# Kernel optimization log

Hardware: AMD Instinct MI355X
Metric: run time of the kernel (lower is better)

Reference implementation:

```python
import jax, jax.numpy as jnp
import numpy as np

HIDDEN_DIM = 2048
NUM_EXPERTS = 64
TOP_K = 2
NUM_TOKENS = 16384


def setup_inputs() -> dict:
    key = jax.random.key(0)
    kx, kw, kb = jax.random.split(key, 3)
    X = jax.random.normal(kx, (NUM_TOKENS, HIDDEN_DIM), dtype=jnp.float32)
    # nn.Linear(hidden_dim, num_experts): weight [num_experts, hidden_dim], bias [num_experts]
    bound = 1.0 / np.sqrt(HIDDEN_DIM)
    W = jax.random.uniform(kw, (NUM_EXPERTS, HIDDEN_DIM), minval=-bound, maxval=bound, dtype=jnp.float32)
    b = jax.random.uniform(kb, (NUM_EXPERTS,), minval=-bound, maxval=bound, dtype=jnp.float32)
    return {"X": X, "W": W, "b": b}


def reference(X, W, b):
    # router_logits = gate(X): [T, E]
    router_logits = jnp.einsum("th,eh->te", X, W) + b
    # softmax in float32 (matches dtype=torch.float)
    routing_probs = jax.nn.softmax(router_logits.astype(jnp.float32), axis=-1)
    # top-k over experts: [T, K]
    router_weights, selected_experts = jax.lax.top_k(routing_probs, TOP_K)
    # renormalize over selected experts (sum cast to X.dtype, result stays fp32 math)
    denom = jnp.sum(router_weights, axis=-1, keepdims=True).astype(X.dtype)
    router_weights = router_weights / denom
    # one-hot expert mask: [T, K, E], int64 like F.one_hot
    expert_mask = jax.nn.one_hot(selected_experts, NUM_EXPERTS, dtype=jnp.int32)
    return (router_logits, router_weights, selected_experts, expert_mask)
```

## Files before the change

### kernel.cpp

```cpp
#include <hip/hip_runtime.h>
#include <math.h>

constexpr int T_TOK = 16384;
constexpr int HDIM  = 2048;
constexpr int NEXP  = 64;
constexpr int TPB   = 64;
constexpr int NWAVE = 8;
constexpr int KPW   = HDIM / NWAVE;
constexpr int KSTEP = 32;
constexpr int NKS   = KPW / KSTEP;

typedef __attribute__((ext_vector_type(8))) short v8s;
typedef __attribute__((ext_vector_type(4))) float v4f;

#define MFMA_BF16 __builtin_amdgcn_mfma_f32_16x16x32_bf16

static __device__ __forceinline__ void split3(float x, unsigned short& h,
                                              unsigned short& m, unsigned short& l)
{
    unsigned u0 = __float_as_uint(x);
    h = (unsigned short)(u0 >> 16);
    float r1 = x - __uint_as_float(u0 & 0xFFFF0000u);
    unsigned u1 = __float_as_uint(r1);
    m = (unsigned short)(u1 >> 16);
    float r2 = r1 - __uint_as_float(u1 & 0xFFFF0000u);
    l = (unsigned short)(__float_as_uint(r2) >> 16);
}

static __device__ __forceinline__ void frag3(const float4& x0, const float4& x1,
                                             v8s& h, v8s& m, v8s& l)
{
    unsigned short sh, sm, sl;
    split3(x0.x, sh, sm, sl); h[0]=(short)sh; m[0]=(short)sm; l[0]=(short)sl;
    split3(x0.y, sh, sm, sl); h[1]=(short)sh; m[1]=(short)sm; l[1]=(short)sl;
    split3(x0.z, sh, sm, sl); h[2]=(short)sh; m[2]=(short)sm; l[2]=(short)sl;
    split3(x0.w, sh, sm, sl); h[3]=(short)sh; m[3]=(short)sm; l[3]=(short)sl;
    split3(x1.x, sh, sm, sl); h[4]=(short)sh; m[4]=(short)sm; l[4]=(short)sl;
    split3(x1.y, sh, sm, sl); h[5]=(short)sh; m[5]=(short)sm; l[5]=(short)sl;
    split3(x1.z, sh, sm, sl); h[6]=(short)sh; m[6]=(short)sm; l[6]=(short)sl;
    split3(x1.w, sh, sm, sl); h[7]=(short)sh; m[7]=(short)sm; l[7]=(short)sl;
}

static __device__ __forceinline__ int swz_e(int tok, int e) {
    return e ^ (((tok >> 2) & 1) << 4);
}

__global__ __launch_bounds__(512, 2)
void moe_router_mfma(const float* __restrict__ X,
                     const float* __restrict__ Wg,
                     const float* __restrict__ Bg,
                     float* __restrict__ out)
{
    __shared__ float red[4][TPB][NEXP];

    const int tid  = threadIdx.x;
    const int lane = tid & 63;
    const int wv   = tid >> 6;
    const int r16  = lane & 15;
    const int q    = lane >> 4;
    const int tok0 = blockIdx.x * TPB;

    const float* pA = X  + (size_t)(tok0 + r16) * HDIM + wv * KPW + q * 8;
    const float* pB = Wg + (size_t)r16 * HDIM + wv * KPW + q * 8;

    v4f acc[4][4];
#pragma unroll
    for (int mt = 0; mt < 4; ++mt)
#pragma unroll
        for (int nt = 0; nt < 4; ++nt)
            acc[mt][nt] = (v4f){0.f, 0.f, 0.f, 0.f};

    float4 a0[4], a1[4], b0[4], b1[4];
#pragma unroll
    for (int mt = 0; mt < 4; ++mt) {
        const float* p = pA + (size_t)mt * 16 * HDIM;
        a0[mt] = *(const float4*)p;
        a1[mt] = *(const float4*)(p + 4);
    }
#pragma unroll
    for (int nt = 0; nt < 4; ++nt) {
        const float* p = pB + (size_t)nt * 16 * HDIM;
        b0[nt] = *(const float4*)p;
        b1[nt] = *(const float4*)(p + 4);
    }

    for (int ks = 0; ks < NKS; ++ks) {
        v8s Ah[4], Am[4], Al[4], Bh[4], Bm[4], Bl[4];
#pragma unroll
        for (int mt = 0; mt < 4; ++mt) frag3(a0[mt], a1[mt], Ah[mt], Am[mt], Al[mt]);
#pragma unroll
        for (int nt = 0; nt < 4; ++nt) frag3(b0[nt], b1[nt], Bh[nt], Bm[nt], Bl[nt]);

        if (ks < NKS - 1) {
            const int off = (ks + 1) * KSTEP;
#pragma unroll
            for (int mt = 0; mt < 4; ++mt) {
                const float* p = pA + (size_t)mt * 16 * HDIM + off;
                a0[mt] = *(const float4*)p;
                a1[mt] = *(const float4*)(p + 4);
            }
#pragma unroll
            for (int nt = 0; nt < 4; ++nt) {
                const float* p = pB + (size_t)nt * 16 * HDIM + off;
                b0[nt] = *(const float4*)p;
                b1[nt] = *(const float4*)(p + 4);
            }
        }

#pragma unroll
        for (int mt = 0; mt < 4; ++mt)
#pragma unroll
            for (int nt = 0; nt < 4; ++nt) {
                v4f a = acc[mt][nt];
                a = MFMA_BF16(Ah[mt], Bh[nt], a, 0, 0, 0);
                a = MFMA_BF16(Ah[mt], Bm[nt], a, 0, 0, 0);
                a = MFMA_BF16(Am[mt], Bh[nt], a, 0, 0, 0);
                a = MFMA_BF16(Ah[mt], Bl[nt], a, 0, 0, 0);
                a = MFMA_BF16(Al[mt], Bh[nt], a, 0, 0, 0);
                a = MFMA_BF16(Am[mt], Bm[nt], a, 0, 0, 0);
                acc[mt][nt] = a;
            }
    }

    if (wv < 4) {
#pragma unroll
        for (int mt = 0; mt < 4; ++mt)
#pragma unroll
            for (int nt = 0; nt < 4; ++nt)
#pragma unroll
                for (int r = 0; r < 4; ++r) {
                    int tok = 16 * mt + q * 4 + r;
                    int e   = 16 * nt + r16;
                    red[wv][tok][swz_e(tok, e)] = acc[mt][nt][r];
                }
    }
    __syncthreads();
    if (wv >= 4) {
#pragma unroll
        for (int mt = 0; mt < 4; ++mt)
#pragma unroll
            for (int nt = 0; nt < 4; ++nt)
#pragma unroll
                for (int r = 0; r < 4; ++r) {
                    int tok = 16 * mt + q * 4 + r;
                    int e   = 16 * nt + r16;
                    red[wv - 4][tok][swz_e(tok, e)] += acc[mt][nt][r];
                }
    }
    __syncthreads();

    if (lane < 8) {
        const int tk = wv * 8 + lane;
        const int t  = tok0 + tk;
        float lg[NEXP];
#pragma unroll
        for (int e = 0; e < NEXP; ++e) {
            int es = swz_e(tk, e);
            lg[e] = ((red[0][tk][es] + red[1][tk][es]) +
                     (red[2][tk][es] + red[3][tk][es])) + Bg[e];
        }
        float* outL = out + (size_t)t * NEXP;
#pragma unroll
        for (int e = 0; e < NEXP; e += 4) {
            float4 v = make_float4(lg[e], lg[e+1], lg[e+2], lg[e+3]);
            *(float4*)(outL + e) = v;
        }
        float mx = lg[0];
#pragma unroll
        for (int e = 1; e < NEXP; ++e) mx = fmaxf(mx, lg[e]);
        float S = 0.f;
#pragma unroll
        for (int e = 0; e < NEXP; ++e) { lg[e] = expf(lg[e] - mx); S += lg[e]; }
#pragma unroll
        for (int e = 0; e < NEXP; ++e) lg[e] = lg[e] / S;

        float v1 = lg[0]; int i1 = 0;
        float v2 = -1.0f; int i2 = 0;
#pragma unroll
        for (int e = 1; e < NEXP; ++e) {
            float rv = lg[e];
            bool g1 = rv > v1;
            bool g2 = rv > v2;
            float nv2 = g1 ? v1 : (g2 ? rv : v2);
            int   ni2 = g1 ? i1 : (g2 ? e  : i2);
            v2 = nv2; i2 = ni2;
            v1 = g1 ? rv : v1;
            i1 = g1 ? e  : i1;
        }
        float den = v1 + v2;
        float w1 = v1 / den, w2 = v2 / den;

        float* outW = out + (size_t)T_TOK * NEXP;
        float* outS = outW + (size_t)T_TOK * 2;
        float* outM = outS + (size_t)T_TOK * 2;
        outW[2*t+0] = w1;        outW[2*t+1] = w2;
        outS[2*t+0] = (float)i1; outS[2*t+1] = (float)i2;

        float* mrow = outM + (size_t)t * 2 * NEXP;
#pragma unroll
        for (int e = 0; e < NEXP; e += 4) {
            float4 a = make_float4(e+0==i1?1.f:0.f, e+1==i1?1.f:0.f,
                                   e+2==i1?1.f:0.f, e+3==i1?1.f:0.f);
            *(float4*)(mrow + e) = a;
            float4 b = make_float4(e+0==i2?1.f:0.f, e+1==i2?1.f:0.f,
                                   e+2==i2?1.f:0.f, e+3==i2?1.f:0.f);
            *(float4*)(mrow + NEXP + e) = b;
        }
    }
}

extern "C" void kernel_launch(void* const* d_in, const int* in_sizes, int n_in,
                              void* d_out, int out_size, void* d_ws, size_t ws_size,
                              hipStream_t stream)
{
    const float* X = (const float*)d_in[0];
    const float* W = (const float*)d_in[1];
    const float* B = (const float*)d_in[2];
    float* out     = (float*)d_out;

    dim3 grid(T_TOK / TPB);
    dim3 block(512);
    hipLaunchKernelGGL(moe_router_mfma, grid, block, 0, stream, X, W, B, out);
}
```

Before: 223.5 us.

## Pre-split W into bf16 planes in a prep kernel and halve tokens per block

```diff
diff --git a/kernel.cpp b/kernel.cpp
--- a/kernel.cpp
+++ b/kernel.cpp
@@ -4,11 +4,12 @@
 constexpr int T_TOK = 16384;
 constexpr int HDIM  = 2048;
 constexpr int NEXP  = 64;
-constexpr int TPB   = 64;
+constexpr int TPB   = 32;
 constexpr int NWAVE = 8;
 constexpr int KPW   = HDIM / NWAVE;
 constexpr int KSTEP = 32;
 constexpr int NKS   = KPW / KSTEP;
+constexpr int WPLANE = NEXP * HDIM;
 
 typedef __attribute__((ext_vector_type(8))) short v8s;
 typedef __attribute__((ext_vector_type(4))) float v4f;
@@ -45,9 +46,24 @@
     return e ^ (((tok >> 2) & 1) << 4);
 }
 
+__global__ __launch_bounds__(256)
+void split_w_kernel(const float* __restrict__ W, unsigned short* __restrict__ ws)
+{
+    int i = blockIdx.x * 256 + threadIdx.x;
+    float4 v = ((const float4*)W)[i];
+    ushort4 h, m, l;
+    split3(v.x, h.x, m.x, l.x);
+    split3(v.y, h.y, m.y, l.y);
+    split3(v.z, h.z, m.z, l.z);
+    split3(v.w, h.w, m.w, l.w);
+    ((ushort4*)(ws           ))[i] = h;
+    ((ushort4*)(ws + WPLANE  ))[i] = m;
+    ((ushort4*)(ws + 2*WPLANE))[i] = l;
+}
+
 __global__ __launch_bounds__(512, 2)
 void moe_router_mfma(const float* __restrict__ X,
-                     const float* __restrict__ Wg,
+                     const unsigned short* __restrict__ Ws,
                      const float* __restrict__ Bg,
                      float* __restrict__ out)
 {
@@ -60,71 +76,71 @@
     const int q    = lane >> 4;
     const int tok0 = blockIdx.x * TPB;
 
-    const float* pA = X  + (size_t)(tok0 + r16) * HDIM + wv * KPW + q * 8;
-    const float* pB = Wg + (size_t)r16 * HDIM + wv * KPW + q * 8;
-
-    v4f acc[4][4];
-#pragma unroll
-    for (int mt = 0; mt < 4; ++mt)
+    const float* pA = X + (size_t)(tok0 + r16) * HDIM + wv * KPW + q * 8;
+    const unsigned short* pBh = Ws + (size_t)r16 * HDIM + wv * KPW + q * 8;
+
+    v4f acc[2][4];
+#pragma unroll
+    for (int mt = 0; mt < 2; ++mt)
 #pragma unroll
         for (int nt = 0; nt < 4; ++nt)
             acc[mt][nt] = (v4f){0.f, 0.f, 0.f, 0.f};
 
-    float4 a0[4], a1[4], b0[4], b1[4];
-#pragma unroll
-    for (int mt = 0; mt < 4; ++mt) {
+    float4 a0[2], a1[2];
+#pragma unroll
+    for (int mt = 0; mt < 2; ++mt) {
         const float* p = pA + (size_t)mt * 16 * HDIM;
         a0[mt] = *(const float4*)p;
         a1[mt] = *(const float4*)(p + 4);
     }
-#pragma unroll
-    for (int nt = 0; nt < 4; ++nt) {
-        const float* p = pB + (size_t)nt * 16 * HDIM;
-        b0[nt] = *(const float4*)p;
-        b1[nt] = *(const float4*)(p + 4);
-    }
 
     for (int ks = 0; ks < NKS; ++ks) {
-        v8s Ah[4], Am[4], Al[4], Bh[4], Bm[4], Bl[4];
-#pragma unroll
-        for (int mt = 0; mt < 4; ++mt) frag3(a0[mt], a1[mt], Ah[mt], Am[mt], Al[mt]);
-#pragma unroll
-        for (int nt = 0; nt < 4; ++nt) frag3(b0[nt], b1[nt], Bh[nt], Bm[nt], Bl[nt]);
+        v8s Ah[2], Am[2], Al[2];
+#pragma unroll
+        for (int mt = 0; mt < 2; ++mt) frag3(a0[mt], a1[mt], Ah[mt], Am[mt], Al[mt]);
 
         if (ks < NKS - 1) {
             const int off = (ks + 1) * KSTEP;
 #pragma unroll
-            for (int mt = 0; mt < 4; ++mt) {
+            for (int mt = 0; mt < 2; ++mt) {
                 const float* p = pA + (size_t)mt * 16 * HDIM + off;
                 a0[mt] = *(const float4*)p;
                 a1[mt] = *(const float4*)(p + 4);
             }
-#pragma unroll
-            for (int nt = 0; nt < 4; ++nt) {
-                const float* p = pB + (size_t)nt * 16 * HDIM + off;
-                b0[nt] = *(const float4*)p;
-                b1[nt] = *(const float4*)(p + 4);
+        }
+
+        const unsigned short* pB = pBh + ks * KSTEP;
+        v8s Bh[2], Bm[2], Bl[2];
+        Bh[0] = *(const v8s*)(pB);
+        Bm[0] = *(const v8s*)(pB + WPLANE);
+        Bl[0] = *(const v8s*)(pB + 2*WPLANE);
+
+#pragma unroll
+        for (int nt = 0; nt < 4; ++nt) {
+            const int c = nt & 1, n2 = c ^ 1;
+            if (nt < 3) {
+                const unsigned short* pn = pB + (size_t)(nt + 1) * 16 * HDIM;
+                Bh[n2] = *(const v8s*)(pn);
+                Bm[n2] = *(const v8s*)(pn + WPLANE);
+                Bl[n2] = *(const v8s*)(pn + 2*WPLANE);
             }
-        }
-
-#pragma unroll
-        for (int mt = 0; mt < 4; ++mt)
-#pragma unroll
-            for (int nt = 0; nt < 4; ++nt) {
+#pragma unroll
+            for (int mt = 0; mt < 2; ++mt) {
                 v4f a = acc[mt][nt];
-                a = MFMA_BF16(Ah[mt], Bh[nt], a, 0, 0, 0);
-                a = MFMA_BF16(Ah[mt], Bm[nt], a, 0, 0, 0);
-                a = MFMA_BF16(Am[mt], Bh[nt], a, 0, 0, 0);
-                a = MFMA_BF16(Ah[mt], Bl[nt], a, 0, 0, 0);
-                a = MFMA_BF16(Al[mt], Bh[nt], a, 0, 0, 0);
-                a = MFMA_BF16(Am[mt], Bm[nt], a, 0, 0, 0);
+                a = MFMA_BF16(Ah[mt], Bh[c], a, 0, 0, 0);
+                a = MFMA_BF16(Ah[mt], Bm[c], a, 0, 0, 0);
+                a = MFMA_BF16(Am[mt], Bh[c], a, 0, 0, 0);
+                a = MFMA_BF16(Ah[mt], Bl[c], a, 0, 0, 0);
+                a = MFMA_BF16(Al[mt], Bh[c], a, 0, 0, 0);
+                a = MFMA_BF16(Am[mt], Bm[c], a, 0, 0, 0);
                 acc[mt][nt] = a;
             }
+        }
     }
 
     if (wv < 4) {
 #pragma unroll
-        for (int mt = 0; mt < 4; ++mt)
+        for (int mt = 0; mt < 2; ++mt)
 #pragma unroll
             for (int nt = 0; nt < 4; ++nt)
 #pragma unroll
@@ -137,7 +153,7 @@
     __syncthreads();
     if (wv >= 4) {
 #pragma unroll
-        for (int mt = 0; mt < 4; ++mt)
+        for (int mt = 0; mt < 2; ++mt)
 #pragma unroll
             for (int nt = 0; nt < 4; ++nt)
 #pragma unroll
@@ -149,8 +165,8 @@
     }
     __syncthreads();
 
-    if (lane < 8) {
-        const int tk = wv * 8 + lane;
+    if (lane < 4) {
+        const int tk = wv * 4 + lane;
         const int t  = tok0 + tk;
         float lg[NEXP];
 #pragma unroll
@@ -217,8 +233,9 @@
     const float* W = (const float*)d_in[1];
     const float* B = (const float*)d_in[2];
     float* out     = (float*)d_out;
-
-    dim3 grid(T_TOK / TPB);
-    dim3 block(512);
-    hipLaunchKernelGGL(moe_router_mfma, grid, block, 0, stream, X, W, B, out);
-}
+    unsigned short* ws = (unsigned short*)d_ws;
+
+    hipLaunchKernelGGL(split_w_kernel, dim3(128), dim3(256), 0, stream, W, ws);
+    hipLaunchKernelGGL(moe_router_mfma, dim3(T_TOK / TPB), dim3(512), 0, stream,
+                       X, ws, B, out);
+}
```

Measured after the change: 260.6 us. 16.6% more time.

## Pre-split gate weights into bf16 fragments and stage them through LDS

Applied to the files above, without the earlier changes.

```diff
diff --git a/kernel.cpp b/kernel.cpp
--- a/kernel.cpp
+++ b/kernel.cpp
@@ -5,10 +5,8 @@
 constexpr int HDIM  = 2048;
 constexpr int NEXP  = 64;
 constexpr int TPB   = 64;
-constexpr int NWAVE = 8;
-constexpr int KPW   = HDIM / NWAVE;
-constexpr int KSTEP = 32;
-constexpr int NKS   = KPW / KSTEP;
+constexpr int NKS   = 32;
+constexpr int KHS   = 32 * 6144;
 
 typedef __attribute__((ext_vector_type(8))) short v8s;
 typedef __attribute__((ext_vector_type(4))) float v4f;
@@ -41,110 +39,146 @@
     split3(x1.w, sh, sm, sl); h[7]=(short)sh; m[7]=(short)sm; l[7]=(short)sl;
 }
 
-static __device__ __forceinline__ int swz_e(int tok, int e) {
-    return e ^ (((tok >> 2) & 1) << 4);
+__global__ __launch_bounds__(256)
+void split_w_frag(const float* __restrict__ W, unsigned short* __restrict__ ws)
+{
+    int idx  = blockIdx.x * 256 + threadIdx.x;
+    int lane = idx & 63;
+    int nt   = (idx >> 6) & 3;
+    int ks   = (idx >> 8) & 31;
+    int kh   = idx >> 13;
+    int e    = nt * 16 + (lane & 15);
+    int k0   = kh * 1024 + ks * 32 + (lane >> 4) * 8;
+    const float* p = W + (size_t)e * HDIM + k0;
+    float4 x0 = *(const float4*)p;
+    float4 x1 = *(const float4*)(p + 4);
+    v8s h, m, l;
+    frag3(x0, x1, h, m, l);
+    size_t bks = (size_t)(kh * 32 + ks) * 6144;
+    *(v8s*)(ws + bks + (0 * 4 + nt) * 512 + lane * 8) = h;
+    *(v8s*)(ws + bks + (1 * 4 + nt) * 512 + lane * 8) = m;
+    *(v8s*)(ws + bks + (2 * 4 + nt) * 512 + lane * 8) = l;
 }
 
 __global__ __launch_bounds__(512, 2)
 void moe_router_mfma(const float* __restrict__ X,
-                     const float* __restrict__ Wg,
+                     const unsigned short* __restrict__ Ws,
                      const float* __restrict__ Bg,
                      float* __restrict__ out)
 {
-    __shared__ float red[4][TPB][NEXP];
+    __shared__ alignas(16) unsigned short Bld[2][24 * 512];
+    float* red = (float*)&Bld[0][0];
 
     const int tid  = threadIdx.x;
     const int lane = tid & 63;
-    const int wv   = tid >> 6;
+    const int wv   = __builtin_amdgcn_readfirstlane(tid >> 6);
     const int r16  = lane & 15;
     const int q    = lane >> 4;
+    const int mt2  = wv & 1;
+    const int nt2  = (wv >> 1) & 1;
+    const int kh   = wv >> 2;
     const int tok0 = blockIdx.x * TPB;
 
-    const float* pA = X  + (size_t)(tok0 + r16) * HDIM + wv * KPW + q * 8;
-    const float* pB = Wg + (size_t)r16 * HDIM + wv * KPW + q * 8;
-
-    v4f acc[4][4];
-#pragma unroll
-    for (int mt = 0; mt < 4; ++mt)
-#pragma unroll
-        for (int nt = 0; nt < 4; ++nt)
-            acc[mt][nt] = (v4f){0.f, 0.f, 0.f, 0.f};
-
-    float4 a0[4], a1[4], b0[4], b1[4];
-#pragma unroll
-    for (int mt = 0; mt < 4; ++mt) {
-        const float* p = pA + (size_t)mt * 16 * HDIM;
-        a0[mt] = *(const float4*)p;
-        a1[mt] = *(const float4*)(p + 4);
-    }
-#pragma unroll
-    for (int nt = 0; nt < 4; ++nt) {
-        const float* p = pB + (size_t)nt * 16 * HDIM;
-        b0[nt] = *(const float4*)p;
-        b1[nt] = *(const float4*)(p + 4);
-    }
-
+    const unsigned short* pWc[3];
+#pragma unroll
+    for (int cc = 0; cc < 3; ++cc) {
+        int c = 3 * wv + cc;
+        pWc[cc] = Ws + (size_t)(c / 12) * KHS + (c % 12) * 512 + lane * 8;
+    }
+
+    const float* pA = X + (size_t)(tok0 + 32 * mt2 + r16) * HDIM + kh * 1024 + q * 8;
+
+    v4f acc[2][2];
+#pragma unroll
+    for (int i = 0; i < 2; ++i)
+#pragma unroll
+        for (int t = 0; t < 2; ++t)
+            acc[i][t] = (v4f){0.f, 0.f, 0.f, 0.f};
+
+    int4 brn[3];
+#pragma unroll
+    for (int cc = 0; cc < 3; ++cc) brn[cc] = *(const int4*)(pWc[cc]);
+#pragma unroll
+    for (int cc = 0; cc < 3; ++cc)
+        *(int4*)&Bld[0][(3 * wv + cc) * 512 + lane * 8] = brn[cc];
+    float4 a0c[2], a1c[2], a0n[2], a1n[2];
+#pragma unroll
+    for (int i = 0; i < 2; ++i) {
+        a0c[i] = *(const float4*)(pA + (size_t)i * 16 * HDIM);
+        a1c[i] = *(const float4*)(pA + (size_t)i * 16 * HDIM + 4);
+    }
+    __syncthreads();
+
+#pragma unroll 2
     for (int ks = 0; ks < NKS; ++ks) {
-        v8s Ah[4], Am[4], Al[4], Bh[4], Bm[4], Bl[4];
-#pragma unroll
-        for (int mt = 0; mt < 4; ++mt) frag3(a0[mt], a1[mt], Ah[mt], Am[mt], Al[mt]);
-#pragma unroll
-        for (int nt = 0; nt < 4; ++nt) frag3(b0[nt], b1[nt], Bh[nt], Bm[nt], Bl[nt]);
-
-        if (ks < NKS - 1) {
-            const int off = (ks + 1) * KSTEP;
-#pragma unroll
-            for (int mt = 0; mt < 4; ++mt) {
-                const float* p = pA + (size_t)mt * 16 * HDIM + off;
-                a0[mt] = *(const float4*)p;
-                a1[mt] = *(const float4*)(p + 4);
+        const int cur = ks & 1, nxt = cur ^ 1;
+        const int ksn = (ks + 1 < NKS) ? ks + 1 : ks;
+
+#pragma unroll
+        for (int cc = 0; cc < 3; ++cc)
+            brn[cc] = *(const int4*)(pWc[cc] + (size_t)ksn * 6144);
+#pragma unroll
+        for (int i = 0; i < 2; ++i) {
+            a0n[i] = *(const float4*)(pA + (size_t)i * 16 * HDIM + ksn * 32);
+            a1n[i] = *(const float4*)(pA + (size_t)i * 16 * HDIM + ksn * 32 + 4);
+        }
+
+        v8s Ah[2], Am[2], Al[2];
+        frag3(a0c[0], a1c[0], Ah[0], Am[0], Al[0]);
+        frag3(a0c[1], a1c[1], Ah[1], Am[1], Al[1]);
+#pragma unroll
+        for (int t = 0; t < 2; ++t) {
+            const int ntl = 2 * nt2 + t;
+            const unsigned short* bp = &Bld[cur][(kh * 12 + ntl) * 512 + lane * 8];
+            v8s Bh = *(const v8s*)(bp);
+            v8s Bm = *(const v8s*)(bp + 4 * 512);
+            v8s Bl = *(const v8s*)(bp + 8 * 512);
+#pragma unroll
+            for (int i = 0; i < 2; ++i) {
+                v4f a = acc[i][t];
+                a = MFMA_BF16(Ah[i], Bh, a, 0, 0, 0);
+                a = MFMA_BF16(Ah[i], Bm, a, 0, 0, 0);
+                a = MFMA_BF16(Am[i], Bh, a, 0, 0, 0);
+                a = MFMA_BF16(Ah[i], Bl, a, 0, 0, 0);
+                a = MFMA_BF16(Al[i], Bh, a, 0, 0, 0);
+                a = MFMA_BF16(Am[i], Bm, a, 0, 0, 0);
+                acc[i][t] = a;
             }
-#pragma unroll
-            for (int nt = 0; nt < 4; ++nt) {
-                const float* p = pB + (size_t)nt * 16 * HDIM + off;
-                b0[nt] = *(const float4*)p;
-                b1[nt] = *(const float4*)(p + 4);
-            }
-        }
-
-#pragma unroll
-        for (int mt = 0; mt < 4; ++mt)
-#pragma unroll
-            for (int nt = 0; nt < 4; ++nt) {
-                v4f a = acc[mt][nt];
-                a = MFMA_BF16(Ah[mt], Bh[nt], a, 0, 0, 0);
-                a = MFMA_BF16(Ah[mt], Bm[nt], a, 0, 0, 0);
-                a = MFMA_BF16(Am[mt], Bh[nt], a, 0, 0, 0);
-                a = MFMA_BF16(Ah[mt], Bl[nt], a, 0, 0, 0);
-                a = MFMA_BF16(Al[mt], Bh[nt], a, 0, 0, 0);
-                a = MFMA_BF16(Am[mt], Bm[nt], a, 0, 0, 0);
-                acc[mt][nt] = a;
-            }
-    }
-
-    if (wv < 4) {
-#pragma unroll
-        for (int mt = 0; mt < 4; ++mt)
-#pragma unroll
-            for (int nt = 0; nt < 4; ++nt)
+        }
+
+        if (ks + 1 < NKS) {
+#pragma unroll
+            for (int cc = 0; cc < 3; ++cc)
+                *(int4*)&Bld[nxt][(3 * wv + cc) * 512 + lane * 8] = brn[cc];
+        }
+#pragma unroll
+        for (int i = 0; i < 2; ++i) { a0c[i] = a0n[i]; a1c[i] = a1n[i]; }
+        __syncthreads();
+    }
+
+    if (kh == 0) {
+#pragma unroll
+        for (int i = 0; i < 2; ++i)
+#pragma unroll
+            for (int t = 0; t < 2; ++t)
 #pragma unroll
                 for (int r = 0; r < 4; ++r) {
-                    int tok = 16 * mt + q * 4 + r;
-                    int e   = 16 * nt + r16;
-                    red[wv][tok][swz_e(tok, e)] = acc[mt][nt][r];
+                    int tok = 32 * mt2 + 16 * i + q * 4 + r;
+                    int e   = (2 * nt2 + t) * 16 + r16;
+                    red[tok * 68 + e] = acc[i][t][r];
                 }
     }
     __syncthreads();
-    if (wv >= 4) {
-#pragma unroll
-        for (int mt = 0; mt < 4; ++mt)
-#pragma unroll
-            for (int nt = 0; nt < 4; ++nt)
+    if (kh == 1) {
+#pragma unroll
+        for (int i = 0; i < 2; ++i)
+#pragma unroll
+            for (int t = 0; t < 2; ++t)
 #pragma unroll
                 for (int r = 0; r < 4; ++r) {
-                    int tok = 16 * mt + q * 4 + r;
-                    int e   = 16 * nt + r16;
-                    red[wv - 4][tok][swz_e(tok, e)] += acc[mt][nt][r];
+                    int tok = 32 * mt2 + 16 * i + q * 4 + r;
+                    int e   = (2 * nt2 + t) * 16 + r16;
+                    red[tok * 68 + e] += acc[i][t][r];
                 }
     }
     __syncthreads();
@@ -154,10 +188,11 @@
         const int t  = tok0 + tk;
         float lg[NEXP];
 #pragma unroll
-        for (int e = 0; e < NEXP; ++e) {
-            int es = swz_e(tk, e);
-            lg[e] = ((red[0][tk][es] + red[1][tk][es]) +
-                     (red[2][tk][es] + red[3][tk][es])) + Bg[e];
+        for (int e = 0; e < NEXP; e += 4) {
+            float4 v  = *(const float4*)&red[tk * 68 + e];
+            float4 bb = *(const float4*)&Bg[e];
+            lg[e+0] = v.x + bb.x; lg[e+1] = v.y + bb.y;
+            lg[e+2] = v.z + bb.z; lg[e+3] = v.w + bb.w;
         }
         float* outL = out + (size_t)t * NEXP;
 #pragma unroll
@@ -217,8 +252,9 @@
     const float* W = (const float*)d_in[1];
     const float* B = (const float*)d_in[2];
     float* out     = (float*)d_out;
-
-    dim3 grid(T_TOK / TPB);
-    dim3 block(512);
-    hipLaunchKernelGGL(moe_router_mfma, grid, block, 0, stream, X, W, B, out);
-}
+    unsigned short* ws = (unsigned short*)d_ws;
+
+    hipLaunchKernelGGL(split_w_frag, dim3(64), dim3(256), 0, stream, W, ws);
+    hipLaunchKernelGGL(moe_router_mfma, dim3(T_TOK / TPB), dim3(512), 0, stream,
+                       X, ws, B, out);
+}
```

Result: slower. 242.9 us (+8.7%).
